# Optimization experiments

Hardware: AMD Instinct MI355X
Metric: run time of the kernel (lower is better)

Reference implementation:

```python
import jax, jax.numpy as jnp
import numpy as np
from functools import reduce

N_QUBITS = 12
DIM = 2 ** N_QUBITS  # 4096
BATCH = 512
TWO_PI = 6.283185307179586


def u3_gate(t):
    # Standard U3(theta, phi, lam) single-qubit gate, complex64 2x2.
    th, ph, la = t[0], t[1], t[2]
    c = jnp.cos(th * 0.5).astype(jnp.complex64)
    s = jnp.sin(th * 0.5).astype(jnp.complex64)
    e_la = jnp.exp(1j * la.astype(jnp.complex64))
    e_ph = jnp.exp(1j * ph.astype(jnp.complex64))
    row0 = jnp.stack([c, -e_la * s])
    row1 = jnp.stack([e_ph * s, e_ph * e_la * c])
    return jnp.stack([row0, row1])  # [2,2] complex64


def full_unitary(thetas):
    # Kron product of per-qubit U3 gates -> [2^n, 2^n] complex64,
    # matching U3(*self.thetas) in the original layer.
    gates = [u3_gate(thetas[i]) for i in range(N_QUBITS)]
    return reduce(jnp.kron, gates)


def setup_inputs() -> dict:
    key = jax.random.key(0)
    k1, k2, k3 = jax.random.split(key, 3)
    thetas = jax.random.uniform(k1, (N_QUBITS, 3), dtype=jnp.float32) * TWO_PI
    state_re = jax.random.normal(k2, (BATCH, DIM, 1), dtype=jnp.float32)
    state_im = jax.random.normal(k3, (BATCH, DIM, 1), dtype=jnp.float32)
    return {"thetas": thetas, "state_re": state_re, "state_im": state_im}


def reference(thetas, state_re, state_im):
    U = full_unitary(thetas)                      # [DIM, DIM] complex64
    state = state_re.astype(jnp.complex64) + 1j * state_im.astype(jnp.complex64)
    out = jnp.einsum('ij,bjk->bik', U, state)     # matrix @ inputs, batched
    # Complex output expressed as real/imag concat on last axis: [B, DIM, 2]
    return jnp.concatenate([out.real, out.imag], axis=-1)
```

## Files before the change

### kernel.cpp

```cpp
#include <hip/hip_runtime.h>
#include <math.h>

#define NQ    12
#define DIM   4096
#define BATCH 512

#define PAD2(i) ((i) + 2 * ((i) >> 4))

#define LEVEL(GA, GB, J) do {                                               \
    _Pragma("unroll")                                                       \
    for (int p = 0; p < 4; ++p) {                                           \
        const int r0 = ((p >> (J)) << ((J) + 1)) | (p & ((1 << (J)) - 1));  \
        const int r1 = r0 | (1 << (J));                                     \
        const float ar = x[r0].x, ai = x[r0].y;                             \
        const float br = x[r1].x, bi = x[r1].y;                             \
        x[r0].x = GA.x * ar - GA.y * ai + GA.z * br - GA.w * bi;            \
        x[r0].y = GA.x * ai + GA.y * ar + GA.z * bi + GA.w * br;            \
        x[r1].x = GB.x * ar - GB.y * ai + GB.z * br - GB.w * bi;            \
        x[r1].y = GB.x * ai + GB.y * ar + GB.z * bi + GB.w * br;            \
    }                                                                       \
} while (0)

#define STAGE(qa, qb, qc) do {                                              \
    const float4 A0 = ((const float4*)g[qa])[0], A1 = ((const float4*)g[qa])[1]; \
    const float4 B0 = ((const float4*)g[qb])[0], B1 = ((const float4*)g[qb])[1]; \
    const float4 C0 = ((const float4*)g[qc])[0], C1 = ((const float4*)g[qc])[1]; \
    LEVEL(A0, A1, 0);                                                       \
    LEVEL(B0, B1, 1);                                                       \
    LEVEL(C0, C1, 2);                                                       \
} while (0)

__global__ __launch_bounds__(512, 4) void u3_apply_kernel(
    const float* __restrict__ thetas,
    const float* __restrict__ sre,
    const float* __restrict__ sim_,
    float*       __restrict__ out)
{
    __shared__ __align__(16) float2 L[4608];
    __shared__ __align__(16) float  g[NQ][8];

    const int b = blockIdx.x;
    const int t = threadIdx.x;

    if (t < NQ) {
        float th = thetas[t * 3 + 0];
        float ph = thetas[t * 3 + 1];
        float la = thetas[t * 3 + 2];
        float c, s, cl, sl, cp, sp;
        __sincosf(th * 0.5f, &s, &c);
        __sincosf(la, &sl, &cl);
        __sincosf(ph, &sp, &cp);
        g[t][0] = c;        g[t][1] = 0.0f;
        g[t][2] = -cl * s;  g[t][3] = -sl * s;
        g[t][4] = cp * s;   g[t][5] = sp * s;
        g[t][6] = (cp * cl - sp * sl) * c;
        g[t][7] = (sp * cl + cp * sl) * c;
    }

    float2 x[8];
    {
        const float4* pre = (const float4*)(sre  + (size_t)b * DIM) + 2 * t;
        const float4* pim = (const float4*)(sim_ + (size_t)b * DIM) + 2 * t;
        float4 vr0 = pre[0], vr1 = pre[1];
        float4 vi0 = pim[0], vi1 = pim[1];
        x[0] = make_float2(vr0.x, vi0.x); x[1] = make_float2(vr0.y, vi0.y);
        x[2] = make_float2(vr0.z, vi0.z); x[3] = make_float2(vr0.w, vi0.w);
        x[4] = make_float2(vr1.x, vi1.x); x[5] = make_float2(vr1.y, vi1.y);
        x[6] = make_float2(vr1.z, vi1.z); x[7] = make_float2(vr1.w, vi1.w);
    }

    __syncthreads();

    STAGE(11, 10, 9);

#pragma unroll
    for (int k = 0; k < 4; ++k) {
        *(float4*)&L[PAD2(8 * t + 2 * k)] =
            make_float4(x[2 * k].x, x[2 * k].y, x[2 * k + 1].x, x[2 * k + 1].y);
    }
    __syncthreads();
    {
        const int base = ((t >> 3) << 6) | (t & 7);
#pragma unroll
        for (int r = 0; r < 8; ++r) x[r] = L[PAD2(base + (r << 3))];
    }

    STAGE(8, 7, 6);

    {
        const int base = ((t >> 3) << 6) | (t & 7);
#pragma unroll
        for (int r = 0; r < 8; ++r) L[PAD2(base + (r << 3))] = x[r];
    }
    __syncthreads();
    {
        const int base = ((t >> 6) << 9) | (t & 63);
#pragma unroll
        for (int r = 0; r < 8; ++r) x[r] = L[PAD2(base + (r << 6))];
    }

    STAGE(5, 4, 3);

    {
        const int base = ((t >> 6) << 9) | (t & 63);
#pragma unroll
        for (int r = 0; r < 8; ++r) L[PAD2(base + (r << 6))] = x[r];
    }
    __syncthreads();
#pragma unroll
    for (int r = 0; r < 8; ++r) x[r] = L[PAD2((r << 9) | t)];

    STAGE(2, 1, 0);

    {
        float2* o2 = (float2*)out + (size_t)b * DIM;
#pragma unroll
        for (int r = 0; r < 8; ++r) o2[(r << 9) | t] = x[r];
    }
}

extern "C" void kernel_launch(void* const* d_in, const int* in_sizes, int n_in,
                              void* d_out, int out_size, void* d_ws, size_t ws_size,
                              hipStream_t stream) {
    const float* thetas = (const float*)d_in[0];
    const float* sre    = (const float*)d_in[1];
    const float* sim_   = (const float*)d_in[2];
    float* out = (float*)d_out;

    u3_apply_kernel<<<BATCH, 512, 0, stream>>>(thetas, sre, sim_, out);
}
```

Baseline: 16.77 us.

## Use 256 threads with 16 amplitudes each, cutting LDS transposes to two

Each thread now holds 16 complex amplitudes and applies four qubit gates per register stage, so the 12 qubits are covered in three stages with two shared-memory exchanges instead of four stages with three. Global loads are issued before gate setup to overlap latency, and output stores use nontemporal hints. This cuts LDS traffic and barriers per block. In exchange it doubles register pressure and halves threads per block, which may reduce occupancy and latency hiding.

New measurement: 16.16 us. 3.6% less time.

```diff
diff --git a/kernel.cpp b/kernel.cpp
--- a/kernel.cpp
+++ b/kernel.cpp
@@ -5,11 +5,15 @@
 #define DIM   4096
 #define BATCH 512
 
+typedef float nt_f2 __attribute__((ext_vector_type(2)));
+
 #define PAD2(i) ((i) + 2 * ((i) >> 4))
 
-#define LEVEL(GA, GB, J) do {                                               \
+#define LEVEL(q, J) do {                                                    \
+    const float4 GA = *(const float4*)&g[q][0];                             \
+    const float4 GB = *(const float4*)&g[q][4];                             \
     _Pragma("unroll")                                                       \
-    for (int p = 0; p < 4; ++p) {                                           \
+    for (int p = 0; p < 8; ++p) {                                           \
         const int r0 = ((p >> (J)) << ((J) + 1)) | (p & ((1 << (J)) - 1));  \
         const int r1 = r0 | (1 << (J));                                     \
         const float ar = x[r0].x, ai = x[r0].y;                             \
@@ -21,16 +25,7 @@
     }                                                                       \
 } while (0)
 
-#define STAGE(qa, qb, qc) do {                                              \
-    const float4 A0 = ((const float4*)g[qa])[0], A1 = ((const float4*)g[qa])[1]; \
-    const float4 B0 = ((const float4*)g[qb])[0], B1 = ((const float4*)g[qb])[1]; \
-    const float4 C0 = ((const float4*)g[qc])[0], C1 = ((const float4*)g[qc])[1]; \
-    LEVEL(A0, A1, 0);                                                       \
-    LEVEL(B0, B1, 1);                                                       \
-    LEVEL(C0, C1, 2);                                                       \
-} while (0)
-
-__global__ __launch_bounds__(512, 4) void u3_apply_kernel(
+__global__ __launch_bounds__(256) void u3_apply_kernel(
     const float* __restrict__ thetas,
     const float* __restrict__ sre,
     const float* __restrict__ sim_,
@@ -41,6 +36,11 @@
 
     const int b = blockIdx.x;
     const int t = threadIdx.x;
+
+    const float4* pre = (const float4*)(sre  + (size_t)b * DIM) + 4 * t;
+    const float4* pim = (const float4*)(sim_ + (size_t)b * DIM) + 4 * t;
+    float4 vr0 = pre[0], vr1 = pre[1], vr2 = pre[2], vr3 = pre[3];
+    float4 vi0 = pim[0], vi1 = pim[1], vi2 = pim[2], vi3 = pim[3];
 
     if (t < NQ) {
         float th = thetas[t * 3 + 0];
@@ -56,66 +56,52 @@
         g[t][6] = (cp * cl - sp * sl) * c;
         g[t][7] = (sp * cl + cp * sl) * c;
     }
-
-    float2 x[8];
-    {
-        const float4* pre = (const float4*)(sre  + (size_t)b * DIM) + 2 * t;
-        const float4* pim = (const float4*)(sim_ + (size_t)b * DIM) + 2 * t;
-        float4 vr0 = pre[0], vr1 = pre[1];
-        float4 vi0 = pim[0], vi1 = pim[1];
-        x[0] = make_float2(vr0.x, vi0.x); x[1] = make_float2(vr0.y, vi0.y);
-        x[2] = make_float2(vr0.z, vi0.z); x[3] = make_float2(vr0.w, vi0.w);
-        x[4] = make_float2(vr1.x, vi1.x); x[5] = make_float2(vr1.y, vi1.y);
-        x[6] = make_float2(vr1.z, vi1.z); x[7] = make_float2(vr1.w, vi1.w);
-    }
-
     __syncthreads();
 
-    STAGE(11, 10, 9);
+    float2 x[16];
+    x[ 0] = make_float2(vr0.x, vi0.x); x[ 1] = make_float2(vr0.y, vi0.y);
+    x[ 2] = make_float2(vr0.z, vi0.z); x[ 3] = make_float2(vr0.w, vi0.w);
+    x[ 4] = make_float2(vr1.x, vi1.x); x[ 5] = make_float2(vr1.y, vi1.y);
+    x[ 6] = make_float2(vr1.z, vi1.z); x[ 7] = make_float2(vr1.w, vi1.w);
+    x[ 8] = make_float2(vr2.x, vi2.x); x[ 9] = make_float2(vr2.y, vi2.y);
+    x[10] = make_float2(vr2.z, vi2.z); x[11] = make_float2(vr2.w, vi2.w);
+    x[12] = make_float2(vr3.x, vi3.x); x[13] = make_float2(vr3.y, vi3.y);
+    x[14] = make_float2(vr3.z, vi3.z); x[15] = make_float2(vr3.w, vi3.w);
+
+    LEVEL(11, 0); LEVEL(10, 1); LEVEL(9, 2); LEVEL(8, 3);
 
 #pragma unroll
-    for (int k = 0; k < 4; ++k) {
-        *(float4*)&L[PAD2(8 * t + 2 * k)] =
+    for (int k = 0; k < 8; ++k) {
+        *(float4*)&L[PAD2((t << 4) | (2 * k))] =
             make_float4(x[2 * k].x, x[2 * k].y, x[2 * k + 1].x, x[2 * k + 1].y);
     }
     __syncthreads();
     {
-        const int base = ((t >> 3) << 6) | (t & 7);
+        const int base = ((t & 0xF0) << 4) | (t & 15);
 #pragma unroll
-        for (int r = 0; r < 8; ++r) x[r] = L[PAD2(base + (r << 3))];
+        for (int r = 0; r < 16; ++r) x[r] = L[PAD2(base | (r << 4))];
     }
 
-    STAGE(8, 7, 6);
+    LEVEL(7, 0); LEVEL(6, 1); LEVEL(5, 2); LEVEL(4, 3);
 
     {
-        const int base = ((t >> 3) << 6) | (t & 7);
+        const int base = ((t & 0xF0) << 4) | (t & 15);
 #pragma unroll
-        for (int r = 0; r < 8; ++r) L[PAD2(base + (r << 3))] = x[r];
-    }
-    __syncthreads();
-    {
-        const int base = ((t >> 6) << 9) | (t & 63);
-#pragma unroll
-        for (int r = 0; r < 8; ++r) x[r] = L[PAD2(base + (r << 6))];
-    }
-
-    STAGE(5, 4, 3);
-
-    {
-        const int base = ((t >> 6) << 9) | (t & 63);
-#pragma unroll
-        for (int r = 0; r < 8; ++r) L[PAD2(base + (r << 6))] = x[r];
+        for (int r = 0; r < 16; ++r) L[PAD2(base | (r << 4))] = x[r];
     }
     __syncthreads();
 #pragma unroll
-    for (int r = 0; r < 8; ++r) x[r] = L[PAD2((r << 9) | t)];
+    for (int r = 0; r < 16; ++r) x[r] = L[PAD2((r << 8) | t)];
 
-    STAGE(2, 1, 0);
+    LEVEL(3, 0); LEVEL(2, 1); LEVEL(1, 2); LEVEL(0, 3);
 
     {
         float2* o2 = (float2*)out + (size_t)b * DIM;
 #pragma unroll
-        for (int r = 0; r < 8; ++r) o2[(r << 9) | t] = x[r];
+        for (int r = 0; r < 16; ++r) {
+            nt_f2 v; v.x = x[r].x; v.y = x[r].y;
+            __builtin_nontemporal_store(v, (nt_f2*)&o2[(r << 8) | t]);
+        }
     }
 }
 
@@ -127,5 +113,5 @@
     const float* sim_   = (const float*)d_in[2];
     float* out = (float*)d_out;
 
-    u3_apply_kernel<<<BATCH, 512, 0, stream>>>(thetas, sre, sim_, out);
+    u3_apply_kernel<<<BATCH, 256, 0, stream>>>(thetas, sre, sim_, out);
 }
```
